# Kernel optimization log

Hardware: AMD Instinct MI355X
Metric: run time of the kernel (lower is better)

Reference implementation:

```python
import jax, jax.numpy as jnp
import numpy as np

B, S, D, H = 2, 2048, 1024, 16
DK = D // H


def setup_inputs() -> dict:
    key = jax.random.key(0)
    ks = jax.random.split(key, 9)
    def xavier(k, shape):
        fan_in, fan_out = shape[1], shape[0]
        lim = jnp.sqrt(6.0 / (fan_in + fan_out))
        return jax.random.uniform(k, shape, jnp.float32, -lim, lim)
    x = jax.random.normal(ks[0], (B, S, D), jnp.float32)
    mask = jnp.ones((B, 1, S), jnp.int32)
    Wq = xavier(ks[1], (D, D)); bq = jnp.zeros((D,), jnp.float32)
    Wk = xavier(ks[2], (D, D)); bk = jnp.zeros((D,), jnp.float32)
    Wv = xavier(ks[3], (D, D)); bv = jnp.zeros((D,), jnp.float32)
    Wo = xavier(ks[4], (D, D)); bo = jnp.zeros((D,), jnp.float32)
    return {"x": x, "mask": mask, "Wq": Wq, "bq": bq, "Wk": Wk, "bk": bk,
            "Wv": Wv, "bv": bv, "Wo": Wo, "bo": bo}


def reference(x, mask, Wq, bq, Wk, bk, Wv, bv, Wo, bo):
    # Linear layers use torch convention y = x @ W.T + b
    q = (x @ Wq.T + bq).reshape(B, S, H, DK).transpose(0, 2, 1, 3)  # [B,H,S,DK]
    k = (x @ Wk.T + bk).reshape(B, S, H, DK).transpose(0, 2, 1, 3)
    v = (x @ Wv.T + bv).reshape(B, S, H, DK).transpose(0, 2, 1, 3)
    scores = jnp.einsum('bhqd,bhkd->bhqk', q, k) / jnp.sqrt(jnp.float32(DK))
    m = mask[:, None, :, :]  # unsqueeze(1): broadcast over heads -> [B,1,1,S]
    scores = jnp.where(m == 0, jnp.float32(-1e9), scores)
    p = jax.nn.softmax(scores, axis=-1)  # dropout p=0.0 -> identity
    ctx = jnp.einsum('bhqk,bhkd->bhqd', p, v)
    ctx = ctx.transpose(0, 2, 1, 3).reshape(B, S, D)
    return ctx @ Wo.T + bo
```

## Files before the change

### kernel.cpp

```cpp
#include <hip/hip_runtime.h>
#include <hip/hip_bf16.h>
#include <math.h>

#define Bn 2
#define Sn 2048
#define Dn 1024
#define Hn 16
#define DKn 64

using fragb  = __attribute__((ext_vector_type(8))) short;
using frag16 = __attribute__((ext_vector_type(8))) _Float16;
using f4     = __attribute__((ext_vector_type(4))) float;

__device__ __forceinline__ short f2bf(float f) {
    union { float f; unsigned u; } v; v.f = f;
    unsigned r = v.u + 0x7FFF + ((v.u >> 16) & 1);
    return (short)(r >> 16);
}
__device__ __forceinline__ float bf2f(short h) {
    union { unsigned u; float f; } v;
    v.u = ((unsigned)(unsigned short)h) << 16;
    return v.f;
}
__device__ __forceinline__ short f2h(float f) {
    _Float16 h = (_Float16)f;
    short s; __builtin_memcpy(&s, &h, 2); return s;
}

#define GLOAD(gptr, lptr)                                                     \
    __builtin_amdgcn_global_load_lds(                                         \
        (const __attribute__((address_space(1))) unsigned int*)(const void*)(gptr), \
        (__attribute__((address_space(3))) unsigned int*)(void*)(lptr), 16, 0, 0)

#define NX (Bn * Sn * Dn)
#define NW (Dn * Dn)

__global__ __launch_bounds__(256) void prep(
    const float* __restrict__ x,  const float* __restrict__ Wq,
    const float* __restrict__ Wk, const float* __restrict__ Wv,
    const float* __restrict__ Wo, const int* __restrict__ mask,
    short* __restrict__ xh,
    short* __restrict__ Wqh, short* __restrict__ Wkh,
    short* __restrict__ Wvh, short* __restrict__ Woh,
    short* __restrict__ mfb)
{
    int i = blockIdx.x * 256 + threadIdx.x;
    const float* src; short* dst; int j;
    if (i < NX)               { src = x;  dst = xh;  j = i; }
    else if (i < NX + NW)     { src = Wq; dst = Wqh; j = i - NX; }
    else if (i < NX + 2 * NW) { src = Wk; dst = Wkh; j = i - NX - NW; }
    else if (i < NX + 3 * NW) { src = Wv; dst = Wvh; j = i - NX - 2 * NW; }
    else if (i < NX + 4 * NW) { src = Wo; dst = Woh; j = i - NX - 3 * NW; }
    else {
        j = i - NX - 4 * NW;
        if (j < Bn * Sn) mfb[j] = mask[j] ? (short)0x3F80 : (short)0;
        return;
    }
    dst[j] = f2h(src[j]);
}

#define BN 128
#define BK 32

template <int BMT>
__global__ __launch_bounds__(256) void gemm_mfma(
    const short* __restrict__ A,
    const short* __restrict__ W0, const float* __restrict__ b0,
    const short* __restrict__ W1, const float* __restrict__ b1,
    const short* __restrict__ W2, const float* __restrict__ b2,
    const int* __restrict__ mask,
    short* __restrict__ Qb, short* __restrict__ Kb, short* __restrict__ Vtb,
    float* __restrict__ outf, int mode)
{
    constexpr int MI = BMT / 32;
    __shared__ __align__(16) short As[BMT * BK];
    __shared__ __align__(16) short Bs[BN * BK];

    const int tid  = threadIdx.x;
    const int wave = tid >> 6;
    const int lane = tid & 63;
    const int quad = lane >> 4;
    const int l16  = lane & 15;
    const int wm   = wave >> 1;
    const int wn   = wave & 1;

    const int m0   = blockIdx.y * BMT;
    const int n0   = blockIdx.x * BN;
    const int widx = n0 >> 10;
    const int nl0  = n0 & 1023;

    const short* Wp   = widx == 0 ? W0 : (widx == 1 ? W1 : W2);
    const float* bias = widx == 0 ? b0 : (widx == 1 ? b1 : b2);

    f4 acc[MI][4];
    #pragma unroll
    for (int i = 0; i < MI; i++)
        #pragma unroll
        for (int j = 0; j < 4; j++) {
            acc[i][j][0] = 0.f; acc[i][j][1] = 0.f;
            acc[i][j][2] = 0.f; acc[i][j][3] = 0.f;
        }

    const int K = Dn;
    const int lrow = tid >> 2;
    const int lkc  = ((tid & 3) ^ ((tid >> 4) & 3)) * 8;
    const short* Ar = A  + (size_t)(m0  + lrow) * K + lkc;
    const short* Br = Wp + (size_t)(nl0 + lrow) * K + lkc;

    const int sw = (l16 >> 2) & 3;
    const int ca = ((quad ^ sw) * 8);

    for (int k0 = 0; k0 < K; k0 += BK) {
        __syncthreads();
        GLOAD(Ar + k0, &As[wave * 512]);
        if constexpr (BMT == 128)
            GLOAD(Ar + (size_t)64 * K + k0, &As[2048 + wave * 512]);
        GLOAD(Br + k0, &Bs[wave * 512]);
        GLOAD(Br + (size_t)64 * K + k0, &Bs[2048 + wave * 512]);
        __syncthreads();

        frag16 a[MI], b[4];
        #pragma unroll
        for (int mi = 0; mi < MI; mi++)
            a[mi] = *(const frag16*)&As[(wm * (BMT / 2) + mi * 16 + l16) * BK + ca];
        #pragma unroll
        for (int ni = 0; ni < 4; ni++)
            b[ni] = *(const frag16*)&Bs[(wn * 64 + ni * 16 + l16) * BK + ca];
        #pragma unroll
        for (int mi = 0; mi < MI; mi++)
            #pragma unroll
            for (int ni = 0; ni < 4; ni++)
                acc[mi][ni] = __builtin_amdgcn_mfma_f32_16x16x32_f16(
                    a[mi], b[ni], acc[mi][ni], 0, 0, 0);
    }

    const float QSCALE = 0.125f * 1.44269504088896340736f;

    #pragma unroll
    for (int mi = 0; mi < MI; mi++) {
        #pragma unroll
        for (int ni = 0; ni < 4; ni++) {
            int nl = nl0 + wn * 64 + ni * 16 + l16;
            float bv = bias[nl];
            #pragma unroll
            for (int r = 0; r < 4; r++) {
                int m = m0 + wm * (BMT / 2) + mi * 16 + quad * 4 + r;
                float v = acc[mi][ni][r] + bv;
                if (mode == 0) {
                    int b  = m >> 11, s = m & (Sn - 1);
                    int h  = nl >> 6, dk = nl & 63;
                    if (widx == 0)
                        Qb[((size_t)(b * Hn + h) * Sn + s) * DKn + dk] = f2bf(v * QSCALE);
                    else if (widx == 1)
                        Kb[((size_t)(b * Hn + h) * Sn + s) * DKn + dk] = f2bf(v);
                    else {
                        float mv = (float)mask[b * Sn + s];
                        Vtb[((size_t)(b * Hn + h) * DKn + dk) * Sn + s] = f2bf(v * mv);
                    }
                } else {
                    outf[(size_t)m * Dn + nl] = v;
                }
            }
        }
    }
}

#define LDK 72
#define LP  72

__global__ __launch_bounds__(256) void attn_mfma(
    const short* __restrict__ Qb, const short* __restrict__ Kb,
    const short* __restrict__ Vtb, const short* __restrict__ mfb,
    short* __restrict__ ctxh)
{
    __shared__ short Ks[64 * LDK];
    __shared__ short Vs[64 * LDK];
    __shared__ short Ps[4][16 * LP];
    __shared__ __align__(16) short mfs[64];

    const int tid  = threadIdx.x;
    const int wave = tid >> 6;
    const int lane = tid & 63;
    const int quad = lane >> 4;
    const int l16  = lane & 15;

    const int qt  = blockIdx.x & 31;
    const int bhh = blockIdx.x >> 5;
    const int b   = bhh >> 4;
    const int h   = bhh & 15;

    const int qrow = qt * 64 + wave * 16 + l16;
    const short* qptr = Qb + ((size_t)bhh * Sn + qrow) * DKn + quad * 8;
    const fragb qf0 = *(const fragb*)(qptr);
    const fragb qf1 = *(const fragb*)(qptr + 32);

    f4 ctx[4];
    #pragma unroll
    for (int dt = 0; dt < 4; dt++) { ctx[dt][0] = 0.f; ctx[dt][1] = 0.f; ctx[dt][2] = 0.f; ctx[dt][3] = 0.f; }
    f4 lacc; lacc[0] = 0.f; lacc[1] = 0.f; lacc[2] = 0.f; lacc[3] = 0.f;

    const short* Kg = Kb  + (size_t)bhh * Sn * DKn;
    const short* Vg = Vtb + (size_t)bhh * DKn * Sn;
    const short* mg = mfb + (size_t)b * Sn;

    for (int kt = 0; kt < Sn / 64; kt++) {
        __syncthreads();
        {
            const uint4* src = (const uint4*)(Kg + (size_t)kt * 64 * DKn);
            #pragma unroll
            for (int c = tid; c < 512; c += 256) {
                int row = c >> 3, col = (c & 7) * 8;
                *(uint4*)&Ks[row * LDK + col] = src[c];
            }
            #pragma unroll
            for (int c = tid; c < 512; c += 256) {
                int d = c >> 3, kc = (c & 7) * 8;
                *(uint4*)&Vs[d * LDK + kc] =
                    *(const uint4*)(Vg + (size_t)d * Sn + kt * 64 + kc);
            }
            if (tid < 8)
                *(uint4*)&mfs[tid * 8] = *(const uint4*)(mg + kt * 64 + tid * 8);
        }
        __syncthreads();

        #pragma unroll
        for (int t = 0; t < 4; t++) {
            fragb k0 = *(const fragb*)&Ks[(t * 16 + l16) * LDK + quad * 8];
            fragb k1 = *(const fragb*)&Ks[(t * 16 + l16) * LDK + quad * 8 + 32];
            f4 a; a[0] = 0.f; a[1] = 0.f; a[2] = 0.f; a[3] = 0.f;
            a = __builtin_amdgcn_mfma_f32_16x16x32_bf16(k0, qf0, a, 0, 0, 0);
            a = __builtin_amdgcn_mfma_f32_16x16x32_bf16(k1, qf1, a, 0, 0, 0);
            unsigned u0 = __float_as_uint(exp2f(a[0]));
            unsigned u1 = __float_as_uint(exp2f(a[1]));
            unsigned u2 = __float_as_uint(exp2f(a[2]));
            unsigned u3 = __float_as_uint(exp2f(a[3]));
            uint2 w;
            w.x = __builtin_amdgcn_perm(u1, u0, 0x07060302u);
            w.y = __builtin_amdgcn_perm(u3, u2, 0x07060302u);
            *(uint2*)&Ps[wave][l16 * LP + 16 * t + quad * 4] = w;
        }

        fragb p0 = *(const fragb*)&Ps[wave][l16 * LP + quad * 8];
        fragb p1 = *(const fragb*)&Ps[wave][l16 * LP + quad * 8 + 32];
        fragb m0 = *(const fragb*)&mfs[quad * 8];
        fragb m1 = *(const fragb*)&mfs[quad * 8 + 32];
        lacc = __builtin_amdgcn_mfma_f32_16x16x32_bf16(p0, m0, lacc, 0, 0, 0);
        lacc = __builtin_amdgcn_mfma_f32_16x16x32_bf16(p1, m1, lacc, 0, 0, 0);
        #pragma unroll
        for (int dt = 0; dt < 4; dt++) {
            fragb v0 = *(const fragb*)&Vs[(dt * 16 + l16) * LDK + quad * 8];
            fragb v1 = *(const fragb*)&Vs[(dt * 16 + l16) * LDK + quad * 8 + 32];
            ctx[dt] = __builtin_amdgcn_mfma_f32_16x16x32_bf16(p0, v0, ctx[dt], 0, 0, 0);
            ctx[dt] = __builtin_amdgcn_mfma_f32_16x16x32_bf16(p1, v1, ctx[dt], 0, 0, 0);
        }
    }

    #pragma unroll
    for (int r = 0; r < 4; r++) {
        float inv = 1.f / lacc[r];
        int row = qt * 64 + wave * 16 + quad * 4 + r;
        #pragma unroll
        for (int dt = 0; dt < 4; dt++) {
            float val = ctx[dt][r] * inv;
            size_t idx = ((size_t)(b * Sn + row)) * Dn + h * DKn + dt * 16 + l16;
            ctxh[idx] = f2h(val);
        }
    }
}

extern "C" void kernel_launch(void* const* d_in, const int* in_sizes, int n_in,
                              void* d_out, int out_size, void* d_ws, size_t ws_size,
                              hipStream_t stream) {
    const float* x    = (const float*)d_in[0];
    const int*   mask = (const int*)d_in[1];
    const float* Wq   = (const float*)d_in[2];
    const float* bq   = (const float*)d_in[3];
    const float* Wk   = (const float*)d_in[4];
    const float* bk   = (const float*)d_in[5];
    const float* Wv   = (const float*)d_in[6];
    const float* bv   = (const float*)d_in[7];
    const float* Wo   = (const float*)d_in[8];
    const float* bo   = (const float*)d_in[9];
    float* out = (float*)d_out;

    char* ws = (char*)d_ws;
    const size_t MB = 1024u * 1024u;
    short* xh  = (short*)(ws + 0 * MB);
    short* Wqh = (short*)(ws + 8 * MB);
    short* Wkh = (short*)(ws + 10 * MB);
    short* Wvh = (short*)(ws + 12 * MB);
    short* Woh = (short*)(ws + 14 * MB);
    short* Qb  = (short*)(ws + 16 * MB);
    short* Kb  = (short*)(ws + 24 * MB);
    short* Vtb = (short*)(ws + 32 * MB);
    short* Ch  = (short*)(ws + 40 * MB);
    short* mfb = (short*)(ws + 48 * MB);

    const int TOT = NX + 4 * NW + Bn * Sn;
    prep<<<(TOT + 255) / 256, 256, 0, stream>>>(
        x, Wq, Wk, Wv, Wo, mask, xh, Wqh, Wkh, Wvh, Woh, mfb);

    gemm_mfma<128><<<dim3(24, 32), 256, 0, stream>>>(
        xh, Wqh, bq, Wkh, bk, Wvh, bv, mask,
        Qb, Kb, Vtb, nullptr, 0);

    attn_mfma<<<dim3(Bn * Hn * (Sn / 64)), 256, 0, stream>>>(
        Qb, Kb, Vtb, mfb, Ch);

    gemm_mfma<64><<<dim3(8, 64), 256, 0, stream>>>(
        Ch, Woh, bo, Woh, bo, Woh, bo, mask,
        nullptr, nullptr, nullptr, out, 1);
}
```

Before: 250.0 us.

## Double query rows per attention block and load K/V via swizzled direct-to-LDS loads

```diff
diff --git a/kernel.cpp b/kernel.cpp
--- a/kernel.cpp
+++ b/kernel.cpp
@@ -165,7 +165,6 @@
     }
 }
 
-#define LDK 72
 #define LP  72
 
 __global__ __launch_bounds__(256) void attn_mfma(
@@ -173,9 +172,9 @@
     const short* __restrict__ Vtb, const short* __restrict__ mfb,
     short* __restrict__ ctxh)
 {
-    __shared__ short Ks[64 * LDK];
-    __shared__ short Vs[64 * LDK];
-    __shared__ short Ps[4][16 * LP];
+    __shared__ __align__(16) short Ks[64 * 64];
+    __shared__ __align__(16) short Vs[64 * 64];
+    __shared__ short Ps[4][32 * LP];
     __shared__ __align__(16) short mfs[64];
 
     const int tid  = threadIdx.x;
@@ -184,88 +183,111 @@
     const int quad = lane >> 4;
     const int l16  = lane & 15;
 
-    const int qt  = blockIdx.x & 31;
-    const int bhh = blockIdx.x >> 5;
+    const int qt  = blockIdx.x & 15;
+    const int bhh = blockIdx.x >> 4;
     const int b   = bhh >> 4;
     const int h   = bhh & 15;
 
-    const int qrow = qt * 64 + wave * 16 + l16;
-    const short* qptr = Qb + ((size_t)bhh * Sn + qrow) * DKn + quad * 8;
-    const fragb qf0 = *(const fragb*)(qptr);
-    const fragb qf1 = *(const fragb*)(qptr + 32);
-
-    f4 ctx[4];
-    #pragma unroll
-    for (int dt = 0; dt < 4; dt++) { ctx[dt][0] = 0.f; ctx[dt][1] = 0.f; ctx[dt][2] = 0.f; ctx[dt][3] = 0.f; }
-    f4 lacc; lacc[0] = 0.f; lacc[1] = 0.f; lacc[2] = 0.f; lacc[3] = 0.f;
-
+    fragb qf[2][2];
+    #pragma unroll
+    for (int w = 0; w < 2; w++) {
+        int qrow = qt * 128 + wave * 32 + w * 16 + l16;
+        const short* qptr = Qb + ((size_t)bhh * Sn + qrow) * DKn + quad * 8;
+        qf[w][0] = *(const fragb*)(qptr);
+        qf[w][1] = *(const fragb*)(qptr + 32);
+    }
+
+    f4 ctx[2][4];
+    #pragma unroll
+    for (int w = 0; w < 2; w++)
+        #pragma unroll
+        for (int dt = 0; dt < 4; dt++) {
+            ctx[w][dt][0] = 0.f; ctx[w][dt][1] = 0.f;
+            ctx[w][dt][2] = 0.f; ctx[w][dt][3] = 0.f;
+        }
+    f4 lacc[2];
+    lacc[0][0] = 0.f; lacc[0][1] = 0.f; lacc[0][2] = 0.f; lacc[0][3] = 0.f;
+    lacc[1] = lacc[0];
+
+    const int lr = lane >> 3;
+    const int sc = ((lane & 7) ^ lr) * 8;
     const short* Kg = Kb  + (size_t)bhh * Sn * DKn;
     const short* Vg = Vtb + (size_t)bhh * DKn * Sn;
     const short* mg = mfb + (size_t)b * Sn;
 
+    const short* Ksrc = Kg + (size_t)(wave * 16 + lr) * DKn + sc;
+    const short* Vsrc = Vg + (size_t)(wave * 16 + lr) * Sn + sc;
+
+    const int c0 = ((quad ^ (l16 & 7)) * 8);
+
     for (int kt = 0; kt < Sn / 64; kt++) {
         __syncthreads();
-        {
-            const uint4* src = (const uint4*)(Kg + (size_t)kt * 64 * DKn);
-            #pragma unroll
-            for (int c = tid; c < 512; c += 256) {
-                int row = c >> 3, col = (c & 7) * 8;
-                *(uint4*)&Ks[row * LDK + col] = src[c];
+        GLOAD(Ksrc + (size_t)kt * 4096,             &Ks[(wave * 16) * 64]);
+        GLOAD(Ksrc + (size_t)kt * 4096 + 8 * DKn,   &Ks[(wave * 16 + 8) * 64]);
+        GLOAD(Vsrc + (size_t)kt * 64,               &Vs[(wave * 16) * 64]);
+        GLOAD(Vsrc + (size_t)kt * 64 + 8 * Sn,      &Vs[(wave * 16 + 8) * 64]);
+        if (tid < 8)
+            *(uint4*)&mfs[tid * 8] = *(const uint4*)(mg + kt * 64 + tid * 8);
+        __syncthreads();
+
+        #pragma unroll
+        for (int t = 0; t < 4; t++) {
+            fragb k0 = *(const fragb*)&Ks[(t * 16 + l16) * 64 + c0];
+            fragb k1 = *(const fragb*)&Ks[(t * 16 + l16) * 64 + (c0 ^ 32)];
+            #pragma unroll
+            for (int w = 0; w < 2; w++) {
+                f4 a; a[0] = 0.f; a[1] = 0.f; a[2] = 0.f; a[3] = 0.f;
+                a = __builtin_amdgcn_mfma_f32_16x16x32_bf16(k0, qf[w][0], a, 0, 0, 0);
+                a = __builtin_amdgcn_mfma_f32_16x16x32_bf16(k1, qf[w][1], a, 0, 0, 0);
+                unsigned u0 = __float_as_uint(exp2f(a[0]));
+                unsigned u1 = __float_as_uint(exp2f(a[1]));
+                unsigned u2 = __float_as_uint(exp2f(a[2]));
+                unsigned u3 = __float_as_uint(exp2f(a[3]));
+                uint2 pw;
+                pw.x = __builtin_amdgcn_perm(u1, u0, 0x07060302u);
+                pw.y = __builtin_amdgcn_perm(u3, u2, 0x07060302u);
+                *(uint2*)&Ps[wave][(w * 16 + l16) * LP + 16 * t + quad * 4] = pw;
             }
-            #pragma unroll
-            for (int c = tid; c < 512; c += 256) {
-                int d = c >> 3, kc = (c & 7) * 8;
-                *(uint4*)&Vs[d * LDK + kc] =
-                    *(const uint4*)(Vg + (size_t)d * Sn + kt * 64 + kc);
-            }
-            if (tid < 8)
-                *(uint4*)&mfs[tid * 8] = *(const uint4*)(mg + kt * 64 + tid * 8);
-        }
-        __syncthreads();
-
-        #pragma unroll
-        for (int t = 0; t < 4; t++) {
-            fragb k0 = *(const fragb*)&Ks[(t * 16 + l16) * LDK + quad * 8];
-            fragb k1 = *(const fragb*)&Ks[(t * 16 + l16) * LDK + quad * 8 + 32];
-            f4 a; a[0] = 0.f; a[1] = 0.f; a[2] = 0.f; a[3] = 0.f;
-            a = __builtin_amdgcn_mfma_f32_16x16x32_bf16(k0, qf0, a, 0, 0, 0);
-            a = __builtin_amdgcn_mfma_f32_16x16x32_bf16(k1, qf1, a, 0, 0, 0);
-            unsigned u0 = __float_as_uint(exp2f(a[0]));
-            unsigned u1 = __float_as_uint(exp2f(a[1]));
-            unsigned u2 = __float_as_uint(exp2f(a[2]));
-            unsigned u3 = __float_as_uint(exp2f(a[3]));
-            uint2 w;
-            w.x = __builtin_amdgcn_perm(u1, u0, 0x07060302u);
-            w.y = __builtin_amdgcn_perm(u3, u2, 0x07060302u);
-            *(uint2*)&Ps[wave][l16 * LP + 16 * t + quad * 4] = w;
-        }
-
-        fragb p0 = *(const fragb*)&Ps[wave][l16 * LP + quad * 8];
-        fragb p1 = *(const fragb*)&Ps[wave][l16 * LP + quad * 8 + 32];
+        }
+
+        fragb p[2][2];
+        #pragma unroll
+        for (int w = 0; w < 2; w++) {
+            p[w][0] = *(const fragb*)&Ps[wave][(w * 16 + l16) * LP + quad * 8];
+            p[w][1] = *(const fragb*)&Ps[wave][(w * 16 + l16) * LP + quad * 8 + 32];
+        }
         fragb m0 = *(const fragb*)&mfs[quad * 8];
         fragb m1 = *(const fragb*)&mfs[quad * 8 + 32];
-        lacc = __builtin_amdgcn_mfma_f32_16x16x32_bf16(p0, m0, lacc, 0, 0, 0);
-        lacc = __builtin_amdgcn_mfma_f32_16x16x32_bf16(p1, m1, lacc, 0, 0, 0);
+        #pragma unroll
+        for (int w = 0; w < 2; w++) {
+            lacc[w] = __builtin_amdgcn_mfma_f32_16x16x32_bf16(p[w][0], m0, lacc[w], 0, 0, 0);
+            lacc[w] = __builtin_amdgcn_mfma_f32_16x16x32_bf16(p[w][1], m1, lacc[w], 0, 0, 0);
+        }
         #pragma unroll
         for (int dt = 0; dt < 4; dt++) {
-            fragb v0 = *(const fragb*)&Vs[(dt * 16 + l16) * LDK + quad * 8];
-            fragb v1 = *(const fragb*)&Vs[(dt * 16 + l16) * LDK + quad * 8 + 32];
-            ctx[dt] = __builtin_amdgcn_mfma_f32_16x16x32_bf16(p0, v0, ctx[dt], 0, 0, 0);
-            ctx[dt] = __builtin_amdgcn_mfma_f32_16x16x32_bf16(p1, v1, ctx[dt], 0, 0, 0);
-        }
-    }
-
-    #pragma unroll
-    for (int r = 0; r < 4; r++) {
-        float inv = 1.f / lacc[r];
-        int row = qt * 64 + wave * 16 + quad * 4 + r;
-        #pragma unroll
-        for (int dt = 0; dt < 4; dt++) {
-            float val = ctx[dt][r] * inv;
-            size_t idx = ((size_t)(b * Sn + row)) * Dn + h * DKn + dt * 16 + l16;
-            ctxh[idx] = f2h(val);
-        }
-    }
+            fragb v0 = *(const fragb*)&Vs[(dt * 16 + l16) * 64 + c0];
+            fragb v1 = *(const fragb*)&Vs[(dt * 16 + l16) * 64 + (c0 ^ 32)];
+            #pragma unroll
+            for (int w = 0; w < 2; w++) {
+                ctx[w][dt] = __builtin_amdgcn_mfma_f32_16x16x32_bf16(p[w][0], v0, ctx[w][dt], 0, 0, 0);
+                ctx[w][dt] = __builtin_amdgcn_mfma_f32_16x16x32_bf16(p[w][1], v1, ctx[w][dt], 0, 0, 0);
+            }
+        }
+    }
+
+    #pragma unroll
+    for (int w = 0; w < 2; w++)
+        #pragma unroll
+        for (int r = 0; r < 4; r++) {
+            float inv = 1.f / lacc[w][r];
+            int row = qt * 128 + wave * 32 + w * 16 + quad * 4 + r;
+            #pragma unroll
+            for (int dt = 0; dt < 4; dt++) {
+                float val = ctx[w][dt][r] * inv;
+                size_t idx = ((size_t)(b * Sn + row)) * Dn + h * DKn + dt * 16 + l16;
+                ctxh[idx] = f2h(val);
+            }
+        }
 }
 
 extern "C" void kernel_launch(void* const* d_in, const int* in_sizes, int n_in,
@@ -304,7 +326,7 @@
         xh, Wqh, bq, Wkh, bk, Wvh, bv, mask,
         Qb, Kb, Vtb, nullptr, 0);
 
-    attn_mfma<<<dim3(Bn * Hn * (Sn / 64)), 256, 0, stream>>>(
+    attn_mfma<<<dim3(Bn * Hn * (Sn / 128)), 256, 0, stream>>>(
         Qb, Kb, Vtb, mfb, Ch);
 
     gemm_mfma<64><<<dim3(8, 64), 256, 0, stream>>>(
```

Result: faster. 232.6 us (-7.0%).
